# Performance work log

Hardware: AMD Instinct MI355X
Metric: run time of the kernel (lower is better)

## Reference

```python
import jax, jax.numpy as jnp
import numpy as np

B, S, D, H, L = 2, 2048, 1024, 16, 8
DH = D // H  # head_dim = 64


def setup_inputs() -> dict:
    key = jax.random.key(0)
    ks = jax.random.split(key, 8)
    s = 0.02  # init scale for weights
    return {
        "x": jax.random.normal(ks[0], (B, S, D), jnp.float32),
        "past_keys": jax.random.normal(ks[1], (B, H, S, L, DH), jnp.float32),
        "past_values": jax.random.normal(ks[2], (B, H, S, L, DH), jnp.float32),
        "Wqkv": jax.random.normal(ks[3], (3 * D, D), jnp.float32) * s,
        "bqkv": jnp.zeros((3 * D,), jnp.float32),
        "Wk": jax.random.normal(ks[4], (D, D), jnp.float32) * s,
        "bk": jnp.zeros((D,), jnp.float32),
        "Wv": jax.random.normal(ks[5], (D, D), jnp.float32) * s,
        "bv": jnp.zeros((D,), jnp.float32),
        "Wo": jax.random.normal(ks[6], (D, D), jnp.float32) * s,
        "bo": jnp.zeros((D,), jnp.float32),
    }


def _split_heads(t):
    b, s, _ = t.shape
    return t.reshape(b, s, H, DH).transpose(0, 2, 1, 3)  # [b,h,s,dh]


def reference(x, past_keys, past_values, Wqkv, bqkv, Wk, bk, Wv, bv, Wo, bo):
    # row q/k/v from fused projection
    qkv = x @ Wqkv.T + bqkv
    q, k, v = jnp.split(qkv, 3, axis=-1)
    q, k, v = _split_heads(q), _split_heads(k), _split_heads(v)
    # shared-memory k/v (returned as next-layer cache); q_col == q_row
    k_col = _split_heads(x @ Wk.T + bk)
    v_col = _split_heads(x @ Wv.T + bv)

    scale = 1.0 / np.sqrt(DH).astype(np.float32)
    # causal token-token scores [b,h,s,s]
    tok = jnp.einsum('bhsd,bhtd->bhst', q, k) * scale
    causal = jnp.triu(jnp.ones((S, S), bool), 1)
    tok = jnp.where(causal, -jnp.inf, tok)
    # per-position depth-memory scores [b,h,s,l]
    mem = jnp.einsum('bhsd,bhsld->bhsl', q, past_keys) * scale
    # joint softmax over concatenated [s + l] axis (dropout p=0)
    w = jax.nn.softmax(jnp.concatenate([tok, mem], axis=-1), axis=-1)
    ctx = (jnp.einsum('bhst,bhtd->bhsd', w[..., :S], v)
           + jnp.einsum('bhsl,bhsld->bhsd', w[..., S:], past_values))
    out = ctx.transpose(0, 2, 1, 3).reshape(B, S, D) @ Wo.T + bo
    return out, k_col, v_col
```

## Files before the change

kernel.cpp:

```cpp
#include <hip/hip_runtime.h>
#include <math.h>

#define B_  2
#define S_  2048
#define D_  1024
#define H_  16
#define L_  8
#define DH_ 64

typedef __attribute__((ext_vector_type(8))) short   short8;
typedef __attribute__((ext_vector_type(4))) float   f32x4;
typedef __attribute__((ext_vector_type(8))) unsigned short us8;

static __device__ __forceinline__ unsigned short f2bf(float f) {
    union { float f; unsigned int u; } x; x.f = f;
    unsigned int r = x.u + 0x7FFFu + ((x.u >> 16) & 1u);
    return (unsigned short)(r >> 16);
}
static __device__ __forceinline__ float bf2f(unsigned short u) {
    union { unsigned int u; float f; } x; x.u = ((unsigned int)u) << 16;
    return x.f;
}
static __device__ __forceinline__ void glds16(const void* g, void* l) {
    __builtin_amdgcn_global_load_lds(
        (const __attribute__((address_space(1))) void*)g,
        (__attribute__((address_space(3))) void*)l, 16, 0, 0);
}

__global__ __launch_bounds__(256) void cvt_bf16(const float* __restrict__ src,
                                                unsigned short* __restrict__ dst,
                                                long n)
{
    const long i = ((long)blockIdx.x * 256 + threadIdx.x) * 8;
    if (i >= n) return;
    const float4 v0 = *(const float4*)(src + i);
    const float4 v1 = *(const float4*)(src + i + 4);
    us8 o;
    o[0] = f2bf(v0.x); o[1] = f2bf(v0.y); o[2] = f2bf(v0.z); o[3] = f2bf(v0.w);
    o[4] = f2bf(v1.x); o[5] = f2bf(v1.y); o[6] = f2bf(v1.z); o[7] = f2bf(v1.w);
    *(us8*)(dst + i) = o;
}

__global__ __launch_bounds__(256) void gemm_bf16(
    const unsigned short* __restrict__ A,
    const unsigned short* __restrict__ Wt,
    const float* __restrict__ bias0,
    const float* __restrict__ bias1,
    const float* __restrict__ bias2,
    void* __restrict__ out,
    float* __restrict__ out2,
    int M, int N, int K, int mode)
{
    __shared__ __align__(16) unsigned short Asm[128 * 32];
    __shared__ __align__(16) unsigned short Bsm[128 * 32];

    const int t  = threadIdx.x;
    const int bm = blockIdx.y * 128;
    const int bn = blockIdx.x * 128;
    const int w = t >> 6, lane = t & 63;
    const int g = lane >> 4, c = lane & 15;
    const int wm = (w & 1) * 64, wn = (w >> 1) * 64;

    const int r0  = t >> 2;
    const int kc0 = (t & 3) ^ ((r0 >> 1) & 3);
    const unsigned short* Ap0 = A  + (long)(bm + r0)      * K + kc0 * 8;
    const unsigned short* Ap1 = A  + (long)(bm + r0 + 64) * K + kc0 * 8;
    const unsigned short* Bp0 = Wt + (long)(bn + r0)      * K + kc0 * 8;
    const unsigned short* Bp1 = Wt + (long)(bn + r0 + 64) * K + kc0 * 8;
    unsigned short* AsD0 = Asm + t * 8;
    unsigned short* AsD1 = Asm + (256 + t) * 8;
    unsigned short* BsD0 = Bsm + t * 8;
    unsigned short* BsD1 = Bsm + (256 + t) * 8;

    const int xv = (c >> 1) & 3;
    int offA[4], offB[4];
#pragma unroll
    for (int i = 0; i < 4; i++) {
        offA[i] = (4 * (wm + i * 16 + c) + (g ^ xv)) * 16;
        offB[i] = (4 * (wn + i * 16 + c) + (g ^ xv)) * 16;
    }

    f32x4 acc[4][4];
#pragma unroll
    for (int i = 0; i < 4; i++)
#pragma unroll
        for (int j = 0; j < 4; j++) { acc[i][j][0]=0.f; acc[i][j][1]=0.f; acc[i][j][2]=0.f; acc[i][j][3]=0.f; }

    for (int k0 = 0; k0 < K; k0 += 32) {
        glds16(Ap0 + k0, AsD0);
        glds16(Ap1 + k0, AsD1);
        glds16(Bp0 + k0, BsD0);
        glds16(Bp1 + k0, BsD1);
        __syncthreads();

        short8 af[4], bf[4];
#pragma unroll
        for (int i = 0; i < 4; i++) af[i] = *(const short8*)((const char*)Asm + offA[i]);
#pragma unroll
        for (int i = 0; i < 4; i++) bf[i] = *(const short8*)((const char*)Bsm + offB[i]);
#pragma unroll
        for (int mt = 0; mt < 4; mt++)
#pragma unroll
            for (int nt = 0; nt < 4; nt++)
                acc[mt][nt] = __builtin_amdgcn_mfma_f32_16x16x32_bf16(af[mt], bf[nt], acc[mt][nt], 0, 0, 0);
        __syncthreads();
    }

#pragma unroll
    for (int mt = 0; mt < 4; mt++) {
#pragma unroll
        for (int nt = 0; nt < 4; nt++) {
            const int col = bn + wn + nt * 16 + c;
            float bv;
            if (mode == 0)          bv = bias0[col];
            else if (col < 3 * D_)  bv = bias0[col];
            else if (col < 4 * D_)  bv = bias1[col - 3 * D_];
            else                    bv = bias2[col - 4 * D_];
            const int row0 = bm + wm + mt * 16 + g * 4;
#pragma unroll
            for (int reg = 0; reg < 4; reg++) {
                const float val = acc[mt][nt][reg] + bv;
                const int rr = row0 + reg;
                if (mode == 0) {
                    ((float*)out)[(long)rr * N + col] = val;
                } else if (col < 3 * D_) {
                    ((unsigned short*)out)[(long)rr * (3 * D_) + col] = f2bf(val);
                } else {
                    const int cc  = col - 3 * D_;
                    const int seg = cc >> 10;
                    const int hh  = (cc >> 6) & 15;
                    const int d   = cc & 63;
                    const int b2 = rr >> 11, s2 = rr & 2047;
                    out2[(long)seg * ((long)B_ * H_ * S_ * DH_)
                         + (((long)(b2 * H_ + hh)) * S_ + s2) * DH_ + d] = val;
                }
            }
        }
    }
}

__global__ __launch_bounds__(256) void prepass(const unsigned short* __restrict__ qkvb,
                                               unsigned short* __restrict__ Kb,
                                               unsigned short* __restrict__ Vtb)
{
    __shared__ __align__(16) unsigned short tile[64][72];
    const int bi = blockIdx.x;
    const int st = bi & 31;
    const int bh = bi >> 5;
    const int b = bh >> 4, h = bh & 15;
    const int t = threadIdx.x;
    const int s_l = t >> 2;
    const int ch = (t & 3) * 16;

    const unsigned short* src = qkvb + (long)(b * S_ + st * 64 + s_l) * (3 * D_) + h * DH_;

    {
        us8 k0 = *(const us8*)(src + D_ + ch);
        us8 k1 = *(const us8*)(src + D_ + ch + 8);
        us8* kd = (us8*)(Kb + ((long)bh * S_ + st * 64 + s_l) * DH_ + ch);
        kd[0] = k0; kd[1] = k1;
    }
    {
        us8 v0 = *(const us8*)(src + 2 * D_ + ch);
        us8 v1 = *(const us8*)(src + 2 * D_ + ch + 8);
        *(us8*)&tile[s_l][ch] = v0;
        *(us8*)&tile[s_l][ch + 8] = v1;
    }
    __syncthreads();
    {
        const int d_l = t >> 2;
        const int sch = (t & 3) * 16;
        us8 o0, o1;
#pragma unroll
        for (int i = 0; i < 8; i++) o0[i] = tile[sch + i][d_l];
#pragma unroll
        for (int i = 0; i < 8; i++) o1[i] = tile[sch + 8 + i][d_l];
        us8* dst = (us8*)(Vtb + ((long)bh * DH_ + d_l) * S_ + st * 64 + sch);
        dst[0] = o0; dst[1] = o1;
    }
}

__global__ __launch_bounds__(128, 4) void attn_mfma(
    const unsigned short* __restrict__ qkvb,
    const unsigned short* __restrict__ Kb,
    const unsigned short* __restrict__ Vtb,
    const float* __restrict__ pk,
    const float* __restrict__ pv,
    unsigned short* __restrict__ ctxb)
{
    __shared__ float msc[2][16][8];
    __shared__ __align__(16) unsigned short Pl[2][16][72];

    const int bi  = blockIdx.x;
    const int bh  = bi & 31;
    const int idx = bi >> 5;
    const int qt  = ((idx & 1) << 5) | ((idx & 2) << 3) | ((idx & 4) << 1)
                  | ((idx & 8) >> 1) | ((idx & 16) >> 3) | ((idx & 32) >> 5);
    const int b = bh >> 4, h = bh & 15;
    const int w = threadIdx.x >> 6;
    const int lane = threadIdx.x & 63;
    const int g = lane >> 4, c = lane & 15;
    const int qrow0 = qt * 32 + w * 16;
    const int dr    = qrow0 & 63;
    const int tEnd  = qrow0 & ~63;
    const float scale = 0.125f;

    const unsigned short* qp = qkvb + ((long)(b * S_) + qrow0 + c) * (3 * D_) + h * DH_;
    const short8 qa0 = *(const short8*)(qp + g * 8);
    const short8 qa1 = *(const short8*)(qp + 32 + g * 8);

    float m[4], lsum[4];
    f32x4 O[4];
#pragma unroll
    for (int f = 0; f < 4; f++) { O[f][0]=0.f; O[f][1]=0.f; O[f][2]=0.f; O[f][3]=0.f; }
#pragma unroll
    for (int reg = 0; reg < 4; reg++) { m[reg] = -INFINITY; lsum[reg] = 0.0f; }

    const unsigned short* Kh = Kb + (long)bh * S_ * DH_;
    const unsigned short* Vh = Vtb + (long)bh * DH_ * S_;

    for (int t0 = 0; t0 <= tEnd; t0 += 64) {
        f32x4 sc[4];
#pragma unroll
        for (int nt = 0; nt < 4; nt++) {
            const unsigned short* kp = Kh + ((long)(t0 + nt * 16 + c)) * DH_ + g * 8;
            const short8 kb0 = *(const short8*)kp;
            const short8 kb1 = *(const short8*)(kp + 32);
            f32x4 a; a[0]=0.f; a[1]=0.f; a[2]=0.f; a[3]=0.f;
            a = __builtin_amdgcn_mfma_f32_16x16x32_bf16(qa0, kb0, a, 0, 0, 0);
            a = __builtin_amdgcn_mfma_f32_16x16x32_bf16(qa1, kb1, a, 0, 0, 0);
#pragma unroll
            for (int reg = 0; reg < 4; reg++) a[reg] *= scale;
            sc[nt] = a;
        }
        if (t0 == tEnd) {
#pragma unroll
            for (int nt = 0; nt < 4; nt++)
#pragma unroll
                for (int reg = 0; reg < 4; reg++)
                    sc[nt][reg] = (nt * 16 + c > dr + g * 4 + reg) ? -INFINITY : sc[nt][reg];
        }
        short8 vb0[4], vb1[4];
#pragma unroll
        for (int nt = 0; nt < 4; nt++) {
            const unsigned short* vp = Vh + ((long)(nt * 16 + c)) * S_ + t0 + g * 8;
            vb0[nt] = *(const short8*)vp;
            vb1[nt] = *(const short8*)(vp + 32);
        }
        float al[4];
#pragma unroll
        for (int reg = 0; reg < 4; reg++) {
            float mx = fmaxf(fmaxf(sc[0][reg], sc[1][reg]), fmaxf(sc[2][reg], sc[3][reg]));
            mx = fmaxf(mx, __shfl_xor(mx, 1));
            mx = fmaxf(mx, __shfl_xor(mx, 2));
            mx = fmaxf(mx, __shfl_xor(mx, 4));
            mx = fmaxf(mx, __shfl_xor(mx, 8));
            const float mn = fmaxf(m[reg], mx);
            const float a  = __expf(m[reg] - mn);
            m[reg] = mn; al[reg] = a;
            float ps = 0.0f;
#pragma unroll
            for (int nt = 0; nt < 4; nt++) {
                float p = __expf(sc[nt][reg] - mn);
                sc[nt][reg] = p; ps += p;
            }
            ps += __shfl_xor(ps, 1); ps += __shfl_xor(ps, 2);
            ps += __shfl_xor(ps, 4); ps += __shfl_xor(ps, 8);
            lsum[reg] = lsum[reg] * a + ps;
        }
#pragma unroll
        for (int f = 0; f < 4; f++)
#pragma unroll
            for (int reg = 0; reg < 4; reg++)
                O[f][reg] *= al[reg];
#pragma unroll
        for (int nt = 0; nt < 4; nt++)
#pragma unroll
            for (int reg = 0; reg < 4; reg++)
                Pl[w][g * 4 + reg][nt * 16 + c] = f2bf(sc[nt][reg]);
        asm volatile("s_waitcnt lgkmcnt(0)" ::: "memory");
        const short8 pa0 = *(const short8*)&Pl[w][c][g * 8];
        const short8 pa1 = *(const short8*)&Pl[w][c][32 + g * 8];
#pragma unroll
        for (int nt = 0; nt < 4; nt++) {
            O[nt] = __builtin_amdgcn_mfma_f32_16x16x32_bf16(pa0, vb0[nt], O[nt], 0, 0, 0);
            O[nt] = __builtin_amdgcn_mfma_f32_16x16x32_bf16(pa1, vb1[nt], O[nt], 0, 0, 0);
        }
    }

    {
        const int r0 = lane >> 3, l0 = lane & 7;
#pragma unroll
        for (int pass = 0; pass < 2; pass++) {
            const int r = r0 + pass * 8;
            const unsigned short* qr = qkvb + ((long)(b * S_) + qrow0 + r) * (3 * D_) + h * DH_;
            const float4* k4 = (const float4*)(pk + (((long)bh * S_ + qrow0 + r) * L_ + l0) * DH_);
            float d = 0.0f;
#pragma unroll
            for (int i = 0; i < 8; i++) {
                const us8 q8 = *(const us8*)(qr + i * 8);
                const float4 ka = k4[2 * i], kb2 = k4[2 * i + 1];
                d += bf2f(q8[0]) * ka.x  + bf2f(q8[1]) * ka.y
                   + bf2f(q8[2]) * ka.z  + bf2f(q8[3]) * ka.w
                   + bf2f(q8[4]) * kb2.x + bf2f(q8[5]) * kb2.y
                   + bf2f(q8[6]) * kb2.z + bf2f(q8[7]) * kb2.w;
            }
            msc[w][r][l0] = d * scale;
        }
    }
    asm volatile("s_waitcnt lgkmcnt(0)" ::: "memory");
#pragma unroll
    for (int reg = 0; reg < 4; reg++) {
        const int r = g * 4 + reg;
        float s8[8];
#pragma unroll
        for (int l = 0; l < 8; l++) s8[l] = msc[w][r][l];
        float mx = s8[0];
#pragma unroll
        for (int l = 1; l < 8; l++) mx = fmaxf(mx, s8[l]);
        const float mn = fmaxf(m[reg], mx);
        const float a  = __expf(m[reg] - mn);
        float p8[8]; float ls = 0.0f;
#pragma unroll
        for (int l = 0; l < 8; l++) { p8[l] = __expf(s8[l] - mn); ls += p8[l]; }
        const float rl = 1.0f / (lsum[reg] * a + ls);
        const float* pvr = pv + ((long)bh * S_ + qrow0 + r) * (L_ * DH_) + c;
        float acc4[4] = {0.f, 0.f, 0.f, 0.f};
#pragma unroll
        for (int l = 0; l < 8; l++)
#pragma unroll
            for (int f = 0; f < 4; f++)
                acc4[f] += p8[l] * pvr[l * DH_ + f * 16];
        unsigned short* op = ctxb + ((long)(b * S_) + qrow0 + r) * D_ + h * DH_ + c;
#pragma unroll
        for (int f = 0; f < 4; f++)
            op[f * 16] = f2bf((O[f][reg] * a + acc4[f]) * rl);
    }
}

extern "C" void kernel_launch(void* const* d_in, const int* in_sizes, int n_in,
                              void* d_out, int out_size, void* d_ws, size_t ws_size,
                              hipStream_t stream)
{
    const float* x    = (const float*)d_in[0];
    const float* pk   = (const float*)d_in[1];
    const float* pv   = (const float*)d_in[2];
    const float* Wqkv = (const float*)d_in[3];
    const float* bqkv = (const float*)d_in[4];
    const float* Wk   = (const float*)d_in[5];
    const float* bk   = (const float*)d_in[6];
    const float* Wv   = (const float*)d_in[7];
    const float* bv   = (const float*)d_in[8];
    const float* Wo   = (const float*)d_in[9];
    const float* bo   = (const float*)d_in[10];

    float* out   = (float*)d_out;
    float* k_col = out + (long)B_ * S_ * D_;

    const int M = B_ * S_;
    const long MD = (long)M * D_;

    unsigned short* xb    = (unsigned short*)d_ws;
    unsigned short* Wqkvb = xb + MD;
    unsigned short* Wkb   = Wqkvb + 3L * D_ * D_;
    unsigned short* Wvb   = Wkb + (long)D_ * D_;
    unsigned short* Wob   = Wvb + (long)D_ * D_;
    unsigned short* qkvb  = Wob + (long)D_ * D_;
    unsigned short* Kb    = qkvb + 3 * MD;
    unsigned short* Vtb   = Kb + MD;
    unsigned short* ctxb  = Vtb + MD;

    dim3 blk(256);

    cvt_bf16<<<dim3((int)(MD / 2048)), blk, 0, stream>>>(x, xb, MD);
    cvt_bf16<<<dim3((int)(3L * D_ * D_ / 2048)), blk, 0, stream>>>(Wqkv, Wqkvb, 3L * D_ * D_);
    cvt_bf16<<<dim3((int)((long)D_ * D_ / 2048)), blk, 0, stream>>>(Wk, Wkb, (long)D_ * D_);
    cvt_bf16<<<dim3((int)((long)D_ * D_ / 2048)), blk, 0, stream>>>(Wv, Wvb, (long)D_ * D_);
    cvt_bf16<<<dim3((int)((long)D_ * D_ / 2048)), blk, 0, stream>>>(Wo, Wob, (long)D_ * D_);

    gemm_bf16<<<dim3(5 * D_ / 128, M / 128), blk, 0, stream>>>(
        xb, Wqkvb, bqkv, bk, bv, qkvb, k_col, M, 5 * D_, D_, 1);
    prepass<<<dim3(B_ * H_ * (S_ / 64)), blk, 0, stream>>>(qkvb, Kb, Vtb);
    attn_mfma<<<dim3(B_ * H_ * (S_ / 32)), dim3(128), 0, stream>>>(qkvb, Kb, Vtb, pk, pv, ctxb);
    gemm_bf16<<<dim3(D_ / 128, M / 128), blk, 0, stream>>>(
        ctxb, Wob, bo, nullptr, nullptr, out, nullptr, M, D_, D_, 0);
}
```

Measured before the change: 615.0 us.

## Double-buffer K tiles, skip softmax rescale lazily, defer row-sum reduction

Prefetches the next K tile into a second register set while the current tile is processed, so global-load latency overlaps with MFMA and softmax work. The online softmax now skips the max reduction and the O rescale when every lane's new max stays within 8 of the running max. The per-row sum is kept per lane and reduced across lanes once after the loop instead of every tile. This uses more registers, so launch bounds drop to 2 blocks per SM, which may lower occupancy.

```diff
diff --git a/kernel.cpp b/kernel.cpp
--- a/kernel.cpp
+++ b/kernel.cpp
@@ -180,7 +180,97 @@
     }
 }
 
-__global__ __launch_bounds__(128, 4) void attn_mfma(
+#define LOAD_KTILE(K0, K1, TT) do {                                         \
+    _Pragma("unroll")                                                       \
+    for (int nt_ = 0; nt_ < 4; nt_++) {                                     \
+        const unsigned short* kp_ = Kh + ((long)((TT) + nt_ * 16 + c)) * DH_ + g * 8; \
+        K0[nt_] = *(const short8*)kp_;                                      \
+        K1[nt_] = *(const short8*)(kp_ + 32);                               \
+    }                                                                       \
+} while (0)
+
+#define ATTN_TILE(TT, K0, K1) do {                                          \
+    const int t0_ = (TT);                                                   \
+    short8 vv0_[4], vv1_[4];                                                \
+    _Pragma("unroll")                                                       \
+    for (int nt_ = 0; nt_ < 4; nt_++) {                                     \
+        const unsigned short* vp_ = Vh + ((long)(nt_ * 16 + c)) * S_ + t0_ + g * 8; \
+        vv0_[nt_] = *(const short8*)vp_;                                    \
+        vv1_[nt_] = *(const short8*)(vp_ + 32);                             \
+    }                                                                       \
+    f32x4 sc_[4];                                                           \
+    _Pragma("unroll")                                                       \
+    for (int nt_ = 0; nt_ < 4; nt_++) {                                     \
+        f32x4 a_; a_[0]=0.f; a_[1]=0.f; a_[2]=0.f; a_[3]=0.f;               \
+        a_ = __builtin_amdgcn_mfma_f32_16x16x32_bf16(qa0, K0[nt_], a_, 0, 0, 0); \
+        a_ = __builtin_amdgcn_mfma_f32_16x16x32_bf16(qa1, K1[nt_], a_, 0, 0, 0); \
+        _Pragma("unroll")                                                   \
+        for (int r_ = 0; r_ < 4; r_++) a_[r_] *= scale;                     \
+        sc_[nt_] = a_;                                                      \
+    }                                                                       \
+    if (t0_ == tEnd) {                                                      \
+        _Pragma("unroll")                                                   \
+        for (int nt_ = 0; nt_ < 4; nt_++)                                   \
+            _Pragma("unroll")                                               \
+            for (int r_ = 0; r_ < 4; r_++)                                  \
+                sc_[nt_][r_] = (nt_ * 16 + c > dr + g * 4 + r_) ? -INFINITY : sc_[nt_][r_]; \
+    }                                                                       \
+    float al_[4]; bool resc_ = false;                                       \
+    _Pragma("unroll")                                                       \
+    for (int r_ = 0; r_ < 4; r_++) {                                        \
+        const float mx_ = fmaxf(fmaxf(sc_[0][r_], sc_[1][r_]),              \
+                                fmaxf(sc_[2][r_], sc_[3][r_]));             \
+        if (__all(mx_ <= m[r_] + 8.0f)) {                                   \
+            al_[r_] = 1.0f;                                                 \
+            float ps_ = 0.0f;                                               \
+            _Pragma("unroll")                                               \
+            for (int nt_ = 0; nt_ < 4; nt_++) {                             \
+                const float p_ = __expf(sc_[nt_][r_] - m[r_]);              \
+                sc_[nt_][r_] = p_; ps_ += p_;                               \
+            }                                                               \
+            lsum_l[r_] += ps_;                                              \
+        } else {                                                            \
+            resc_ = true;                                                   \
+            float M_ = mx_;                                                 \
+            M_ = fmaxf(M_, __shfl_xor(M_, 1));                              \
+            M_ = fmaxf(M_, __shfl_xor(M_, 2));                              \
+            M_ = fmaxf(M_, __shfl_xor(M_, 4));                              \
+            M_ = fmaxf(M_, __shfl_xor(M_, 8));                              \
+            const float mn_ = fmaxf(m[r_], M_);                             \
+            const float a_ = __expf(m[r_] - mn_);                           \
+            m[r_] = mn_; al_[r_] = a_;                                      \
+            float ps_ = 0.0f;                                               \
+            _Pragma("unroll")                                               \
+            for (int nt_ = 0; nt_ < 4; nt_++) {                             \
+                const float p_ = __expf(sc_[nt_][r_] - mn_);                \
+                sc_[nt_][r_] = p_; ps_ += p_;                               \
+            }                                                               \
+            lsum_l[r_] = lsum_l[r_] * a_ + ps_;                             \
+        }                                                                   \
+    }                                                                       \
+    if (resc_) {                                                            \
+        _Pragma("unroll")                                                   \
+        for (int f_ = 0; f_ < 4; f_++)                                      \
+            _Pragma("unroll")                                               \
+            for (int r_ = 0; r_ < 4; r_++)                                  \
+                O[f_][r_] *= al_[r_];                                       \
+    }                                                                       \
+    _Pragma("unroll")                                                       \
+    for (int nt_ = 0; nt_ < 4; nt_++)                                       \
+        _Pragma("unroll")                                                   \
+        for (int r_ = 0; r_ < 4; r_++)                                      \
+            Pl[w][g * 4 + r_][nt_ * 16 + c] = f2bf(sc_[nt_][r_]);           \
+    asm volatile("s_waitcnt lgkmcnt(0)" ::: "memory");                      \
+    const short8 pa0_ = *(const short8*)&Pl[w][c][g * 8];                   \
+    const short8 pa1_ = *(const short8*)&Pl[w][c][32 + g * 8];              \
+    _Pragma("unroll")                                                       \
+    for (int nt_ = 0; nt_ < 4; nt_++) {                                     \
+        O[nt_] = __builtin_amdgcn_mfma_f32_16x16x32_bf16(pa0_, vv0_[nt_], O[nt_], 0, 0, 0); \
+        O[nt_] = __builtin_amdgcn_mfma_f32_16x16x32_bf16(pa1_, vv1_[nt_], O[nt_], 0, 0, 0); \
+    }                                                                       \
+} while (0)
+
+__global__ __launch_bounds__(128, 2) void attn_mfma(
     const unsigned short* __restrict__ qkvb,
     const unsigned short* __restrict__ Kb,
     const unsigned short* __restrict__ Vtb,
@@ -209,83 +299,37 @@
     const short8 qa0 = *(const short8*)(qp + g * 8);
     const short8 qa1 = *(const short8*)(qp + 32 + g * 8);
 
-    float m[4], lsum[4];
+    float m[4], lsum_l[4];
     f32x4 O[4];
 #pragma unroll
     for (int f = 0; f < 4; f++) { O[f][0]=0.f; O[f][1]=0.f; O[f][2]=0.f; O[f][3]=0.f; }
 #pragma unroll
-    for (int reg = 0; reg < 4; reg++) { m[reg] = -INFINITY; lsum[reg] = 0.0f; }
+    for (int reg = 0; reg < 4; reg++) { m[reg] = -INFINITY; lsum_l[reg] = 0.0f; }
 
     const unsigned short* Kh = Kb + (long)bh * S_ * DH_;
     const unsigned short* Vh = Vtb + (long)bh * DH_ * S_;
 
-    for (int t0 = 0; t0 <= tEnd; t0 += 64) {
-        f32x4 sc[4];
-#pragma unroll
-        for (int nt = 0; nt < 4; nt++) {
-            const unsigned short* kp = Kh + ((long)(t0 + nt * 16 + c)) * DH_ + g * 8;
-            const short8 kb0 = *(const short8*)kp;
-            const short8 kb1 = *(const short8*)(kp + 32);
-            f32x4 a; a[0]=0.f; a[1]=0.f; a[2]=0.f; a[3]=0.f;
-            a = __builtin_amdgcn_mfma_f32_16x16x32_bf16(qa0, kb0, a, 0, 0, 0);
-            a = __builtin_amdgcn_mfma_f32_16x16x32_bf16(qa1, kb1, a, 0, 0, 0);
-#pragma unroll
-            for (int reg = 0; reg < 4; reg++) a[reg] *= scale;
-            sc[nt] = a;
-        }
-        if (t0 == tEnd) {
-#pragma unroll
-            for (int nt = 0; nt < 4; nt++)
-#pragma unroll
-                for (int reg = 0; reg < 4; reg++)
-                    sc[nt][reg] = (nt * 16 + c > dr + g * 4 + reg) ? -INFINITY : sc[nt][reg];
-        }
-        short8 vb0[4], vb1[4];
-#pragma unroll
-        for (int nt = 0; nt < 4; nt++) {
-            const unsigned short* vp = Vh + ((long)(nt * 16 + c)) * S_ + t0 + g * 8;
-            vb0[nt] = *(const short8*)vp;
-            vb1[nt] = *(const short8*)(vp + 32);
-        }
-        float al[4];
-#pragma unroll
-        for (int reg = 0; reg < 4; reg++) {
-            float mx = fmaxf(fmaxf(sc[0][reg], sc[1][reg]), fmaxf(sc[2][reg], sc[3][reg]));
-            mx = fmaxf(mx, __shfl_xor(mx, 1));
-            mx = fmaxf(mx, __shfl_xor(mx, 2));
-            mx = fmaxf(mx, __shfl_xor(mx, 4));
-            mx = fmaxf(mx, __shfl_xor(mx, 8));
-            const float mn = fmaxf(m[reg], mx);
-            const float a  = __expf(m[reg] - mn);
-            m[reg] = mn; al[reg] = a;
-            float ps = 0.0f;
-#pragma unroll
-            for (int nt = 0; nt < 4; nt++) {
-                float p = __expf(sc[nt][reg] - mn);
-                sc[nt][reg] = p; ps += p;
-            }
-            ps += __shfl_xor(ps, 1); ps += __shfl_xor(ps, 2);
-            ps += __shfl_xor(ps, 4); ps += __shfl_xor(ps, 8);
-            lsum[reg] = lsum[reg] * a + ps;
-        }
-#pragma unroll
-        for (int f = 0; f < 4; f++)
-#pragma unroll
-            for (int reg = 0; reg < 4; reg++)
-                O[f][reg] *= al[reg];
-#pragma unroll
-        for (int nt = 0; nt < 4; nt++)
-#pragma unroll
-            for (int reg = 0; reg < 4; reg++)
-                Pl[w][g * 4 + reg][nt * 16 + c] = f2bf(sc[nt][reg]);
-        asm volatile("s_waitcnt lgkmcnt(0)" ::: "memory");
-        const short8 pa0 = *(const short8*)&Pl[w][c][g * 8];
-        const short8 pa1 = *(const short8*)&Pl[w][c][32 + g * 8];
-#pragma unroll
-        for (int nt = 0; nt < 4; nt++) {
-            O[nt] = __builtin_amdgcn_mfma_f32_16x16x32_bf16(pa0, vb0[nt], O[nt], 0, 0, 0);
-            O[nt] = __builtin_amdgcn_mfma_f32_16x16x32_bf16(pa1, vb1[nt], O[nt], 0, 0, 0);
-        }
+    short8 kA0[4], kA1[4], kB0[4], kB1[4];
+    LOAD_KTILE(kA0, kA1, 0);
+    int t0 = 0;
+    for (;;) {
+        if (t0 + 64 <= tEnd) LOAD_KTILE(kB0, kB1, t0 + 64);
+        ATTN_TILE(t0, kA0, kA1);
+        if (t0 == tEnd) break;
+        t0 += 64;
+        if (t0 + 64 <= tEnd) LOAD_KTILE(kA0, kA1, t0 + 64);
+        ATTN_TILE(t0, kB0, kB1);
+        if (t0 == tEnd) break;
+        t0 += 64;
+    }
+
+    float lsum[4];
+#pragma unroll
+    for (int reg = 0; reg < 4; reg++) {
+        float s = lsum_l[reg];
+        s += __shfl_xor(s, 1); s += __shfl_xor(s, 2);
+        s += __shfl_xor(s, 4); s += __shfl_xor(s, 8);
+        lsum[reg] = s;
     }
 
     {
```

New measurement: 567.2 us. 7.8% less time.
